# Optimization experiments

Measured on AMD Instinct MI355X. Metric: run time of the kernel, lower is better.

Reference implementation:

```python
import jax, jax.numpy as jnp
import numpy as np
import math

B, L, H, E = 16, 512, 8, 64


def setup_inputs() -> dict:
    key = jax.random.key(0)
    k0, k1, k2, k3 = jax.random.split(key, 4)
    return {
        "queries": jax.random.normal(k0, (B, L, H, E), jnp.float32),
        "keys": jax.random.normal(k1, (B, L, H, E), jnp.float32),
        "values": jax.random.normal(k2, (B, L, H, E), jnp.float32),
        "sigma": jax.random.normal(k3, (B, L, H), jnp.float32),
        "attn_mask": jnp.zeros((B, L, L), dtype=bool),  # unused: mask_flag=False
    }


def reference(queries, keys, values, sigma, attn_mask):
    # queries/keys: [B,L,H,E], values: [B,S,H,D], sigma: [B,L,H]
    Edim = queries.shape[-1]
    scale = 1.0 / math.sqrt(Edim)
    scores = jnp.einsum("blhe,bshe->bhls", queries, keys)
    attn = scale * scores  # mask_flag=False -> no causal mask

    # learned sigma -> positive bandwidth in (1e-5, 2]
    sig = jnp.transpose(sigma, (0, 2, 1))  # [B,H,L]
    sig = jax.nn.sigmoid(sig * 5.0) + 1e-5
    sig = jnp.power(3.0, sig) - 1.0
    sig = sig[..., None]  # [B,H,L,1]

    win = attn.shape[-1]
    idx = jnp.arange(win)
    dist = jnp.abs(idx[:, None] - idx[None, :]).astype(attn.dtype)  # |i-j|, [L,L]
    inv_sqrt_2pi = 1.0 / math.sqrt(2.0 * math.pi)
    prior = inv_sqrt_2pi / sig * jnp.exp(-(dist ** 2) / (2.0 * sig ** 2))  # [B,H,L,L]

    series = jax.nn.softmax(attn, axis=-1)  # dropout p=0.0 -> identity
    V = jnp.einsum("bhls,bshd->blhd", series, values)
    sigma_full = jnp.broadcast_to(sig, prior.shape)
    # output_attention=True
    return V, series, prior, sigma_full
```

## Files before the change

kernel.cpp:

```cpp
#include <hip/hip_runtime.h>
#include <hip/hip_bf16.h>
#include <math.h>

#define B_ 16
#define L_ 512
#define H_ 8
#define E_ 64

typedef float f32x4 __attribute__((ext_vector_type(4)));
typedef short bf16x8 __attribute__((ext_vector_type(8)));
typedef short s16x4 __attribute__((ext_vector_type(4)));
typedef unsigned int u32x2 __attribute__((ext_vector_type(2)));
typedef unsigned int u32x4 __attribute__((ext_vector_type(4)));

__device__ __forceinline__ short f2bf(float f) {
    __hip_bfloat16 h = __float2bfloat16(f);
    return __builtin_bit_cast(short, h);
}

__device__ __forceinline__ bf16x8 cvt8(const float* p) {
    f32x4 a = *(const f32x4*)p;
    f32x4 b = *(const f32x4*)(p + 4);
    bf16x8 r;
    r[0] = f2bf(a[0]); r[1] = f2bf(a[1]); r[2] = f2bf(a[2]); r[3] = f2bf(a[3]);
    r[4] = f2bf(b[0]); r[5] = f2bf(b[1]); r[6] = f2bf(b[2]); r[7] = f2bf(b[3]);
    return r;
}

__global__ void vt_kernel(const float* __restrict__ V, unsigned short* __restrict__ Vt) {
    __shared__ float tile[64][68];
    int bid = blockIdx.x;
    int sc = bid & 7, bh = bid >> 3;
    int h = bh & 7, b = bh >> 3;
    int t = threadIdx.x;
    int s0 = sc * 64;
    const float* vb = V + ((size_t)b * 512 + s0) * 512 + h * 64;
    #pragma unroll
    for (int i = 0; i < 4; ++i) {
        int srow = i * 16 + (t >> 4);
        int d4 = (t & 15) * 4;
        f32x4 v = *(const f32x4*)(vb + (size_t)srow * 512 + d4);
        tile[srow][d4 + 0] = v[0]; tile[srow][d4 + 1] = v[1];
        tile[srow][d4 + 2] = v[2]; tile[srow][d4 + 3] = v[3];
    }
    __syncthreads();
    int d = t >> 2, c = t & 3;
    unsigned us[8];
    #pragma unroll
    for (int k = 0; k < 8; ++k) {
        unsigned lo = (unsigned short)f2bf(tile[c * 16 + 2 * k][d]);
        unsigned hi = (unsigned short)f2bf(tile[c * 16 + 2 * k + 1][d]);
        us[k] = lo | (hi << 16);
    }
    unsigned short* dst = Vt + ((size_t)bh * 64 + d) * 512 + s0 + c * 16;
    *(u32x4*)dst       = u32x4{us[0], us[1], us[2], us[3]};
    *(u32x4*)(dst + 8) = u32x4{us[4], us[5], us[6], us[7]};
}

#define PSTR 544
#define WLDS (16 * PSTR * 2 + 64)

__launch_bounds__(256, 2)
__global__ void attn_kernel(const float* __restrict__ Qg,
                            const float* __restrict__ Kg,
                            const unsigned short* __restrict__ Vt,
                            float* __restrict__ Vout,
                            float* __restrict__ series) {
    __shared__ __align__(16) char lds[4 * WLDS];
    int tid = threadIdx.x;
    int w = tid >> 6, l = tid & 63;
    int lm = l & 15, g = l >> 4;

    int bid = blockIdx.x;
    int nid = (bid & 7) * 128 + (bid >> 3);
    int rb = nid & 7, bh = nid >> 3;
    int h = bh & 7, b = bh >> 3;
    int l0 = rb * 64 + w * 16;

    char* wl = lds + w * WLDS;

    const float* qrow = Qg + ((size_t)b * 512 + l0 + lm) * 512 + h * 64;
    bf16x8 qf0 = cvt8(qrow + g * 8);
    bf16x8 qf1 = cvt8(qrow + 32 + g * 8);

    const float* krow0 = Kg + (size_t)b * 512 * 512 + (size_t)lm * 512 + h * 64 + g * 8;
    f32x4 acc[32];
    #pragma unroll
    for (int t = 0; t < 32; ++t) acc[t] = 0.0f;
    #pragma unroll
    for (int t = 0; t < 32; ++t) {
        const float* kr = krow0 + (size_t)t * 16 * 512;
        bf16x8 kf0 = cvt8(kr);
        bf16x8 kf1 = cvt8(kr + 32);
        acc[t] = __builtin_amdgcn_mfma_f32_16x16x32_bf16(kf0, qf0, acc[t], 0, 0, 0);
        acc[t] = __builtin_amdgcn_mfma_f32_16x16x32_bf16(kf1, qf1, acc[t], 0, 0, 0);
    }

    float m = -1e30f;
    #pragma unroll
    for (int t = 0; t < 32; ++t)
        m = fmaxf(m, fmaxf(fmaxf(acc[t][0], acc[t][1]), fmaxf(acc[t][2], acc[t][3])));
    m = fmaxf(m, __shfl_xor(m, 16));
    m = fmaxf(m, __shfl_xor(m, 32));
    const float SC = 0.125f * 1.44269504088896340736f;
    float ssum = 0.0f;
    #pragma unroll
    for (int t = 0; t < 32; ++t) {
        #pragma unroll
        for (int r = 0; r < 4; ++r) {
            float p = exp2f((acc[t][r] - m) * SC);
            acc[t][r] = p;
            ssum += p;
        }
    }
    ssum += __shfl_xor(ssum, 16);
    ssum += __shfl_xor(ssum, 32);
    float inv = 1.0f / ssum;

    #pragma unroll
    for (int t = 0; t < 32; ++t) {
        s16x4 pw;
        pw[0] = f2bf(acc[t][0]); pw[1] = f2bf(acc[t][1]);
        pw[2] = f2bf(acc[t][2]); pw[3] = f2bf(acc[t][3]);
        int off = (lm * (PSTR * 2) + (t * 16 + g * 4) * 2) ^ ((lm & 7) << 4);
        *(s16x4*)(wl + off) = pw;
    }

    f32x4 oacc[4];
    #pragma unroll
    for (int dt = 0; dt < 4; ++dt) oacc[dt] = 0.0f;
    const unsigned short* vtb = Vt + ((size_t)bh * 64 + lm) * 512;
    #pragma unroll
    for (int ks = 0; ks < 16; ++ks) {
        int poff = (lm * (PSTR * 2) + (ks * 32 + g * 8) * 2) ^ ((lm & 7) << 4);
        bf16x8 pb = *(const bf16x8*)(wl + poff);
        #pragma unroll
        for (int dt = 0; dt < 4; ++dt) {
            bf16x8 va = *(const bf16x8*)(vtb + (size_t)dt * 16 * 512 + ks * 32 + g * 8);
            oacc[dt] = __builtin_amdgcn_mfma_f32_16x16x32_bf16(va, pb, oacc[dt], 0, 0, 0);
        }
    }

    float isq = __shfl(inv, l >> 2);
    size_t srow = ((size_t)bh * 512 + l0 + (l >> 2)) * 512;
    int pbase = ((l >> 2) * (PSTR * 2));
    int pswz = (((l >> 2) & 7) << 4);
    #pragma unroll
    for (int j = 0; j < 32; ++j) {
        int s = j * 16 + (l & 3) * 4;
        u32x2 pk = *(const u32x2*)(wl + ((pbase + s * 2) ^ pswz));
        f32x4 o;
        o[0] = __uint_as_float(pk[0] << 16) * isq;
        o[1] = __uint_as_float(pk[0] & 0xffff0000u) * isq;
        o[2] = __uint_as_float(pk[1] << 16) * isq;
        o[3] = __uint_as_float(pk[1] & 0xffff0000u) * isq;
        *(f32x4*)(series + srow + s) = o;
    }

    float* Olds = (float*)wl;
    #pragma unroll
    for (int dt = 0; dt < 4; ++dt)
        #pragma unroll
        for (int r = 0; r < 4; ++r)
            Olds[(dt * 16 + g * 4 + r) * 17 + lm] = oacc[dt][r] * inv;
    #pragma unroll
    for (int it = 0; it < 4; ++it) {
        int rr = it * 4 + g;
        f32x4 o;
        #pragma unroll
        for (int e = 0; e < 4; ++e) o[e] = Olds[(lm * 4 + e) * 17 + rr];
        *(f32x4*)(Vout + ((size_t)b * 512 + l0 + rr) * 512 + h * 64 + lm * 4) = o;
    }
}

__global__ void prior_kernel(const float* __restrict__ sigma,
                             float* __restrict__ prior,
                             float* __restrict__ sigf) {
    int t = threadIdx.x;
    int row = blockIdx.x * 4 + (t >> 6);
    int l = row & 511, bh = row >> 9;
    int h = bh & 7, b = bh >> 3;
    float x = sigma[((size_t)b * 512 + l) * 8 + h];
    float s = 1.0f / (1.0f + exp2f(-7.2134752044448170368f * x)) + 1e-5f;
    float sg = exp2f(s * 1.5849625007211562f) - 1.0f;
    float invc = 0.3989422804014327f / sg;
    float c2 = -0.72134752044448170368f / (sg * sg);
    int c = t & 63;
    size_t base = (size_t)row * 512 + c * 8;
    f32x4 p0, p1, sv;
    #pragma unroll
    for (int k = 0; k < 4; ++k) {
        float d0 = (float)(l - (c * 8 + k));
        float d1 = (float)(l - (c * 8 + 4 + k));
        p0[k] = invc * exp2f(c2 * d0 * d0);
        p1[k] = invc * exp2f(c2 * d1 * d1);
        sv[k] = sg;
    }
    *(f32x4*)(prior + base)     = p0;
    *(f32x4*)(prior + base + 4) = p1;
    *(f32x4*)(sigf + base)      = sv;
    *(f32x4*)(sigf + base + 4)  = sv;
}

extern "C" void kernel_launch(void* const* d_in, const int* in_sizes, int n_in,
                              void* d_out, int out_size, void* d_ws, size_t ws_size,
                              hipStream_t stream) {
    const float* queries = (const float*)d_in[0];
    const float* keys    = (const float*)d_in[1];
    const float* values  = (const float*)d_in[2];
    const float* sigma   = (const float*)d_in[3];

    float* out = (float*)d_out;
    const size_t nV = (size_t)B_ * L_ * H_ * E_;
    const size_t nS = (size_t)B_ * H_ * L_ * L_;
    float* Vout       = out;
    float* series     = out + nV;
    float* prior      = out + nV + nS;
    float* sigma_full = out + nV + 2 * nS;

    unsigned short* Vt = (unsigned short*)sigma_full;

    vt_kernel<<<B_ * H_ * 8, 256, 0, stream>>>(values, Vt);
    attn_kernel<<<B_ * H_ * 8, 256, 0, stream>>>(queries, keys, Vt, Vout, series);
    prior_kernel<<<B_ * H_ * L_ / 4, 256, 0, stream>>>(sigma, prior, sigma_full);
}
```

Before: 535.2 us.

## Fuse prior generation into attention and pre-pack Q/K/V into MFMA fragment layout

Adds a prep kernel that converts Q and K to bf16 in MFMA-fragment order in the workspace, and repacks V into the same fragment layout, so the attention kernel does coalesced 16-byte bf16 loads instead of strided fp32 loads plus conversion. The series output is now written straight from fp32 registers rather than re-read from bf16 LDS, and the prior and sigma_full generation is fused into the attention kernel, which removes a launch. The trade-offs are an extra prep pass over Q and K, uncoalesced row-strided series and prior stores, and more work per thread in the fused kernel.

```diff
diff --git a/kernel.cpp b/kernel.cpp
--- a/kernel.cpp
+++ b/kernel.cpp
@@ -10,7 +10,6 @@
 typedef float f32x4 __attribute__((ext_vector_type(4)));
 typedef short bf16x8 __attribute__((ext_vector_type(8)));
 typedef short s16x4 __attribute__((ext_vector_type(4)));
-typedef unsigned int u32x2 __attribute__((ext_vector_type(2)));
 typedef unsigned int u32x4 __attribute__((ext_vector_type(4)));
 
 __device__ __forceinline__ short f2bf(float f) {
@@ -27,14 +26,32 @@
     return r;
 }
 
-__global__ void vt_kernel(const float* __restrict__ V, unsigned short* __restrict__ Vt) {
+__global__ void qk_prep(const float* __restrict__ Qg, const float* __restrict__ Kg,
+                        unsigned short* __restrict__ Qf, unsigned short* __restrict__ Kf) {
+    int bid = blockIdx.x;
+    int tg = bid & 7, bh = (bid >> 3) & 127, sel = bid >> 10;
+    const float* src = sel ? Kg : Qg;
+    unsigned short* dst = sel ? Kf : Qf;
+    int h = bh & 7, b = bh >> 3;
+    int t = threadIdx.x;
+    int w = t >> 6, l = t & 63, lm = l & 15, g = l >> 4;
+    int tile = tg * 4 + w;
+    int row = tile * 16 + lm;
+    const float* p = src + ((size_t)(b * 512 + row) * 8 + h) * 64 + g * 8;
+    unsigned short* d0 = dst + ((size_t)(bh * 32 + tile) * 2) * 512 + l * 8;
+    bf16x8 v0 = cvt8(p);
+    bf16x8 v1 = cvt8(p + 32);
+    *(bf16x8*)d0        = v0;
+    *(bf16x8*)(d0 + 512) = v1;
+}
+
+__global__ void v_prep(const float* __restrict__ V, unsigned short* __restrict__ Vtf) {
     __shared__ float tile[64][68];
     int bid = blockIdx.x;
     int sc = bid & 7, bh = bid >> 3;
     int h = bh & 7, b = bh >> 3;
     int t = threadIdx.x;
-    int s0 = sc * 64;
-    const float* vb = V + ((size_t)b * 512 + s0) * 512 + h * 64;
+    const float* vb = V + ((size_t)(b * 512 + sc * 64) * 8 + h) * 64;
     #pragma unroll
     for (int i = 0; i < 4; ++i) {
         int srow = i * 16 + (t >> 4);
@@ -44,56 +61,55 @@
         tile[srow][d4 + 2] = v[2]; tile[srow][d4 + 3] = v[3];
     }
     __syncthreads();
-    int d = t >> 2, c = t & 3;
-    unsigned us[8];
-    #pragma unroll
-    for (int k = 0; k < 8; ++k) {
-        unsigned lo = (unsigned short)f2bf(tile[c * 16 + 2 * k][d]);
-        unsigned hi = (unsigned short)f2bf(tile[c * 16 + 2 * k + 1][d]);
-        us[k] = lo | (hi << 16);
-    }
-    unsigned short* dst = Vt + ((size_t)bh * 64 + d) * 512 + s0 + c * 16;
-    *(u32x4*)dst       = u32x4{us[0], us[1], us[2], us[3]};
-    *(u32x4*)(dst + 8) = u32x4{us[4], us[5], us[6], us[7]};
-}
-
-#define PSTR 544
-#define WLDS (16 * PSTR * 2 + 64)
+    int dt = t >> 6, l = t & 63, lm = l & 15, g = l >> 4;
+    #pragma unroll
+    for (int ksl = 0; ksl < 2; ++ksl) {
+        int ks = sc * 2 + ksl;
+        bf16x8 u;
+        #pragma unroll
+        for (int j = 0; j < 8; ++j)
+            u[j] = f2bf(tile[ksl * 32 + g * 8 + j][dt * 16 + lm]);
+        *(bf16x8*)(Vtf + ((size_t)(bh * 4 + dt) * 16 + ks) * 512 + l * 8) = u;
+    }
+}
 
 __launch_bounds__(256, 2)
-__global__ void attn_kernel(const float* __restrict__ Qg,
-                            const float* __restrict__ Kg,
-                            const unsigned short* __restrict__ Vt,
-                            float* __restrict__ Vout,
-                            float* __restrict__ series) {
-    __shared__ __align__(16) char lds[4 * WLDS];
+__global__ void attn_fused(const unsigned short* __restrict__ Qf,
+                           const unsigned short* __restrict__ Kf,
+                           const unsigned short* __restrict__ Vtf,
+                           const float* __restrict__ sigma,
+                           float* __restrict__ Vout,
+                           float* __restrict__ series,
+                           float* __restrict__ prior,
+                           float* __restrict__ sigf) {
+    __shared__ __align__(16) char lds[4 * 16384];
     int tid = threadIdx.x;
-    int w = tid >> 6, l = tid & 63;
-    int lm = l & 15, g = l >> 4;
+    int w = tid >> 6, l = tid & 63, lm = l & 15, g = l >> 4;
 
     int bid = blockIdx.x;
     int nid = (bid & 7) * 128 + (bid >> 3);
     int rb = nid & 7, bh = nid >> 3;
     int h = bh & 7, b = bh >> 3;
-    int l0 = rb * 64 + w * 16;
-
-    char* wl = lds + w * WLDS;
-
-    const float* qrow = Qg + ((size_t)b * 512 + l0 + lm) * 512 + h * 64;
-    bf16x8 qf0 = cvt8(qrow + g * 8);
-    bf16x8 qf1 = cvt8(qrow + 32 + g * 8);
-
-    const float* krow0 = Kg + (size_t)b * 512 * 512 + (size_t)lm * 512 + h * 64 + g * 8;
+    int qt = rb * 4 + w;
+    int l0 = qt * 16;
+
+    char* wl = lds + w * 16384;
+    int swz = (lm & 7) << 4;
+
+    const unsigned short* qfp = Qf + ((size_t)(bh * 32 + qt) * 2) * 512 + l * 8;
+    bf16x8 qf0 = *(const bf16x8*)qfp;
+    bf16x8 qf1 = *(const bf16x8*)(qfp + 512);
+
+    const unsigned short* kfp = Kf + (size_t)bh * 32768 + l * 8;
     f32x4 acc[32];
     #pragma unroll
     for (int t = 0; t < 32; ++t) acc[t] = 0.0f;
     #pragma unroll
     for (int t = 0; t < 32; ++t) {
-        const float* kr = krow0 + (size_t)t * 16 * 512;
-        bf16x8 kf0 = cvt8(kr);
-        bf16x8 kf1 = cvt8(kr + 32);
-        acc[t] = __builtin_amdgcn_mfma_f32_16x16x32_bf16(kf0, qf0, acc[t], 0, 0, 0);
-        acc[t] = __builtin_amdgcn_mfma_f32_16x16x32_bf16(kf1, qf1, acc[t], 0, 0, 0);
+        bf16x8 k0 = *(const bf16x8*)(kfp + t * 1024);
+        bf16x8 k1 = *(const bf16x8*)(kfp + t * 1024 + 512);
+        acc[t] = __builtin_amdgcn_mfma_f32_16x16x32_bf16(k0, qf0, acc[t], 0, 0, 0);
+        acc[t] = __builtin_amdgcn_mfma_f32_16x16x32_bf16(k1, qf1, acc[t], 0, 0, 0);
     }
 
     float m = -1e30f;
@@ -106,55 +122,41 @@
     float ssum = 0.0f;
     #pragma unroll
     for (int t = 0; t < 32; ++t) {
+        f32x4 p;
         #pragma unroll
         for (int r = 0; r < 4; ++r) {
-            float p = exp2f((acc[t][r] - m) * SC);
-            acc[t][r] = p;
-            ssum += p;
+            p[r] = exp2f((acc[t][r] - m) * SC);
+            ssum += p[r];
         }
+        acc[t] = p;
     }
     ssum += __shfl_xor(ssum, 16);
     ssum += __shfl_xor(ssum, 32);
     float inv = 1.0f / ssum;
 
+    float* sp = series + ((size_t)bh * 512 + l0 + lm) * 512 + g * 4;
     #pragma unroll
     for (int t = 0; t < 32; ++t) {
+        f32x4 p = acc[t];
         s16x4 pw;
-        pw[0] = f2bf(acc[t][0]); pw[1] = f2bf(acc[t][1]);
-        pw[2] = f2bf(acc[t][2]); pw[3] = f2bf(acc[t][3]);
-        int off = (lm * (PSTR * 2) + (t * 16 + g * 4) * 2) ^ ((lm & 7) << 4);
-        *(s16x4*)(wl + off) = pw;
+        pw[0] = f2bf(p[0]); pw[1] = f2bf(p[1]); pw[2] = f2bf(p[2]); pw[3] = f2bf(p[3]);
+        *(s16x4*)(wl + (((lm << 10) + 32 * t + 8 * g) ^ swz)) = pw;
+        f32x4 sv; sv[0] = p[0] * inv; sv[1] = p[1] * inv; sv[2] = p[2] * inv; sv[3] = p[3] * inv;
+        *(f32x4*)(sp + t * 16) = sv;
     }
 
     f32x4 oacc[4];
     #pragma unroll
     for (int dt = 0; dt < 4; ++dt) oacc[dt] = 0.0f;
-    const unsigned short* vtb = Vt + ((size_t)bh * 64 + lm) * 512;
+    const unsigned short* vfp = Vtf + (size_t)bh * 32768 + l * 8;
     #pragma unroll
     for (int ks = 0; ks < 16; ++ks) {
-        int poff = (lm * (PSTR * 2) + (ks * 32 + g * 8) * 2) ^ ((lm & 7) << 4);
-        bf16x8 pb = *(const bf16x8*)(wl + poff);
+        bf16x8 pb = *(const bf16x8*)(wl + (((lm << 10) + 64 * ks + 16 * g) ^ swz));
         #pragma unroll
         for (int dt = 0; dt < 4; ++dt) {
-            bf16x8 va = *(const bf16x8*)(vtb + (size_t)dt * 16 * 512 + ks * 32 + g * 8);
+            bf16x8 va = *(const bf16x8*)(vfp + (size_t)(dt * 16 + ks) * 512);
             oacc[dt] = __builtin_amdgcn_mfma_f32_16x16x32_bf16(va, pb, oacc[dt], 0, 0, 0);
         }
-    }
-
-    float isq = __shfl(inv, l >> 2);
-    size_t srow = ((size_t)bh * 512 + l0 + (l >> 2)) * 512;
-    int pbase = ((l >> 2) * (PSTR * 2));
-    int pswz = (((l >> 2) & 7) << 4);
-    #pragma unroll
-    for (int j = 0; j < 32; ++j) {
-        int s = j * 16 + (l & 3) * 4;
-        u32x2 pk = *(const u32x2*)(wl + ((pbase + s * 2) ^ pswz));
-        f32x4 o;
-        o[0] = __uint_as_float(pk[0] << 16) * isq;
-        o[1] = __uint_as_float(pk[0] & 0xffff0000u) * isq;
-        o[2] = __uint_as_float(pk[1] << 16) * isq;
-        o[3] = __uint_as_float(pk[1] & 0xffff0000u) * isq;
-        *(f32x4*)(series + srow + s) = o;
     }
 
     float* Olds = (float*)wl;
@@ -169,37 +171,29 @@
         f32x4 o;
         #pragma unroll
         for (int e = 0; e < 4; ++e) o[e] = Olds[(lm * 4 + e) * 17 + rr];
-        *(f32x4*)(Vout + ((size_t)b * 512 + l0 + rr) * 512 + h * 64 + lm * 4) = o;
-    }
-}
-
-__global__ void prior_kernel(const float* __restrict__ sigma,
-                             float* __restrict__ prior,
-                             float* __restrict__ sigf) {
-    int t = threadIdx.x;
-    int row = blockIdx.x * 4 + (t >> 6);
-    int l = row & 511, bh = row >> 9;
-    int h = bh & 7, b = bh >> 3;
-    float x = sigma[((size_t)b * 512 + l) * 8 + h];
+        *(f32x4*)(Vout + ((size_t)(b * 512 + l0 + rr) * 8 + h) * 64 + lm * 4) = o;
+    }
+
+    int row_l = l0 + lm;
+    float x = sigma[((size_t)b * 512 + row_l) * 8 + h];
     float s = 1.0f / (1.0f + exp2f(-7.2134752044448170368f * x)) + 1e-5f;
-    float sg = exp2f(s * 1.5849625007211562f) - 1.0f;
+    float sg = exp2f(1.5849625007211562f * s) - 1.0f;
     float invc = 0.3989422804014327f / sg;
     float c2 = -0.72134752044448170368f / (sg * sg);
-    int c = t & 63;
-    size_t base = (size_t)row * 512 + c * 8;
-    f32x4 p0, p1, sv;
-    #pragma unroll
-    for (int k = 0; k < 4; ++k) {
-        float d0 = (float)(l - (c * 8 + k));
-        float d1 = (float)(l - (c * 8 + 4 + k));
-        p0[k] = invc * exp2f(c2 * d0 * d0);
-        p1[k] = invc * exp2f(c2 * d1 * d1);
-        sv[k] = sg;
-    }
-    *(f32x4*)(prior + base)     = p0;
-    *(f32x4*)(prior + base + 4) = p1;
-    *(f32x4*)(sigf + base)      = sv;
-    *(f32x4*)(sigf + base + 4)  = sv;
+    size_t pbase = ((size_t)bh * 512 + row_l) * 512 + g * 128;
+    f32x4 sgv; sgv[0] = sg; sgv[1] = sg; sgv[2] = sg; sgv[3] = sg;
+    #pragma unroll
+    for (int c4 = 0; c4 < 32; ++c4) {
+        int j0 = g * 128 + c4 * 4;
+        f32x4 pr;
+        #pragma unroll
+        for (int k = 0; k < 4; ++k) {
+            float d = (float)(row_l - (j0 + k));
+            pr[k] = invc * exp2f(c2 * d * d);
+        }
+        *(f32x4*)(prior + pbase + c4 * 4) = pr;
+        *(f32x4*)(sigf + pbase + c4 * 4) = sgv;
+    }
 }
 
 extern "C" void kernel_launch(void* const* d_in, const int* in_sizes, int n_in,
@@ -218,9 +212,12 @@
     float* prior      = out + nV + nS;
     float* sigma_full = out + nV + 2 * nS;
 
-    unsigned short* Vt = (unsigned short*)sigma_full;
-
-    vt_kernel<<<B_ * H_ * 8, 256, 0, stream>>>(values, Vt);
-    attn_kernel<<<B_ * H_ * 8, 256, 0, stream>>>(queries, keys, Vt, Vout, series);
-    prior_kernel<<<B_ * H_ * L_ / 4, 256, 0, stream>>>(sigma, prior, sigma_full);
-}
+    unsigned short* Qf  = (unsigned short*)d_ws;
+    unsigned short* Kf  = Qf + nV;
+    unsigned short* Vtf = Kf + nV;
+
+    qk_prep<<<2048, 256, 0, stream>>>(queries, keys, Qf, Kf);
+    v_prep<<<1024, 256, 0, stream>>>(values, Vtf);
+    attn_fused<<<1024, 256, 0, stream>>>(Qf, Kf, Vtf, sigma,
+                                         Vout, series, prior, sigma_full);
+}
```

After: 571.8 us. 1.07x slower.
